# Kernel optimization log

Hardware: AMD Instinct MI355X
Metric: run time of the kernel (lower is better)

## Reference

```python
import jax, jax.numpy as jnp
import numpy as np
import math

H = 2048      # hidden_size
NH = 16       # num_attention_heads
HN = H // NH  # head dim = 128
B = 4
S = 2048

def setup_inputs() -> dict:
    key = jax.random.key(0)
    k1, k2, k3, k4, k5 = jax.random.split(key, 5)
    hidden_states = jax.random.normal(k1, (B, S, H), dtype=jnp.float32)
    # causal (left-to-right) multiplicative mask, [1,1,s,s]
    ltor_mask = jnp.tril(jnp.ones((S, S), dtype=jnp.float32))[None, None]
    scale = 0.02
    w_qkv = jax.random.normal(k2, (H, 3 * H), dtype=jnp.float32) * scale
    b_qkv = jnp.zeros((3 * H,), dtype=jnp.float32)
    w_dense = jax.random.normal(k3, (H, H), dtype=jnp.float32) * scale
    b_dense = jnp.zeros((H,), dtype=jnp.float32)
    return {"hidden_states": hidden_states, "ltor_mask": ltor_mask,
            "w_qkv": w_qkv, "b_qkv": b_qkv, "w_dense": w_dense, "b_dense": b_dense}

def reference(hidden_states, ltor_mask, w_qkv, b_qkv, w_dense, b_dense):
    b, s, h = hidden_states.shape
    mixed = hidden_states @ w_qkv + b_qkv                      # [b,s,3h]
    q, k, v = jnp.split(mixed, 3, axis=-1)                     # each [b,s,h]
    def heads(t):
        return t.reshape(b, s, NH, HN).transpose(0, 2, 1, 3)   # [b,np,s,hn]
    q, k, v = heads(q), heads(k), heads(v)
    scores = jnp.einsum('bnqd,bnkd->bnqk', q, k) / math.sqrt(HN)
    scores = scores * ltor_mask - 10000.0 * (1.0 - ltor_mask)
    probs = jax.nn.softmax(scores, axis=-1)
    # dropout probs are 0 -> identity
    ctx = jnp.einsum('bnqk,bnkd->bnqd', probs, v)               # [b,np,s,hn]
    ctx = ctx.transpose(0, 2, 1, 3).reshape(b, s, h)            # [b,s,h]
    out = ctx @ w_dense + b_dense
    return out
```

## Files before the change

### kernel.cpp

```cpp
#include <hip/hip_runtime.h>

#define NHEADS 16
#define HDIM 2048
#define HN 128
#define SS 2048

typedef short short8 __attribute__((ext_vector_type(8)));
typedef __bf16 bf16x8 __attribute__((ext_vector_type(8)));
typedef float f32x4 __attribute__((ext_vector_type(4)));

__device__ __forceinline__ unsigned short f2bf(float f) {
  unsigned int u = __float_as_uint(f);
  u += 0x7FFFu + ((u >> 16) & 1u);
  return (unsigned short)(u >> 16);
}
__device__ __forceinline__ bf16x8 ld8(const void* p) {
  short8 s = *(const short8*)p;
  return __builtin_bit_cast(bf16x8, s);
}
__device__ __forceinline__ void gld_lds16(const void* g, void* l) {
  __builtin_amdgcn_global_load_lds(
      (const __attribute__((address_space(1))) unsigned int*)g,
      (__attribute__((address_space(3))) unsigned int*)l, 16, 0, 0);
}

__global__ __launch_bounds__(256) void cast_bf16_kernel(
    const float* __restrict__ in, unsigned short* __restrict__ out, int n4) {
  int i = blockIdx.x * 256 + threadIdx.x;
  if (i >= n4) return;
  float4 v = ((const float4*)in)[i];
  ushort4 o;
  o.x = f2bf(v.x); o.y = f2bf(v.y); o.z = f2bf(v.z); o.w = f2bf(v.w);
  ((ushort4*)out)[i] = o;
}

__global__ __launch_bounds__(256) void transpose_cast_kernel(
    const float* __restrict__ in, unsigned short* __restrict__ out, int R, int C) {
  __shared__ float tile[64][65];
  int tx = threadIdx.x & 63, ty = threadIdx.x >> 6;
  int c0 = blockIdx.x * 64, r0 = blockIdx.y * 64;
#pragma unroll
  for (int i = 0; i < 16; ++i) {
    int r = ty + i * 4;
    tile[r][tx] = in[(size_t)(r0 + r) * C + (c0 + tx)];
  }
  __syncthreads();
#pragma unroll
  for (int i = 0; i < 16; ++i) {
    int r = ty + i * 4;
    out[(size_t)(c0 + r) * R + (r0 + tx)] = f2bf(tile[tx][r]);
  }
}


#define STAGE_A(bsel, h, kt)                                                      \
  do {                                                                            \
    gld_lds16((const char*)(Ab + (size_t)sa_m[h][0] * K + (size_t)(kt) * 64) +    \
                  scol0,                                                          \
              lds + (bsel) * 65536 + (h) * 16384 + t * 16);                       \
    gld_lds16((const char*)(Ab + (size_t)sa_m[h][1] * K + (size_t)(kt) * 64) +    \
                  scol1,                                                          \
              lds + (bsel) * 65536 + (h) * 16384 + (t + 512) * 16);               \
  } while (0)

#define STAGE_B(bsel, h, kt)                                                      \
  do {                                                                            \
    gld_lds16((const char*)(Bb + (size_t)sb_n[h][0] * K + (size_t)(kt) * 64) +    \
                  scol0,                                                          \
              lds + (bsel) * 65536 + 32768 + (h) * 16384 + t * 16);               \
    gld_lds16((const char*)(Bb + (size_t)sb_n[h][1] * K + (size_t)(kt) * 64) +    \
                  scol1,                                                          \
              lds + (bsel) * 65536 + 32768 + (h) * 16384 + (t + 512) * 16);       \
  } while (0)

#define LDA(bsel, mh)                                                             \
  do {                                                                            \
    _Pragma("unroll") for (int mf = 0; mf < 4; ++mf) {                            \
      int row = mf * 16 + ln15 + wr * 64 + (mh) * 128;                            \
      int sw = (row & 7) << 4;                                                    \
      const char* base = lds + (bsel) * 65536 + row * 128;                        \
      a[mf][0] = ld8(base + ((g * 16) ^ sw));                                     \
      a[mf][1] = ld8(base + ((64 + g * 16) ^ sw));                                \
    }                                                                             \
  } while (0)

#define LDB(bsel, nh, breg)                                                       \
  do {                                                                            \
    _Pragma("unroll") for (int nf = 0; nf < 2; ++nf) {                            \
      int row = nf * 16 + ln15 + wc * 32 + (nh) * 128;                            \
      int sw = (row & 7) << 4;                                                    \
      const char* base = lds + (bsel) * 65536 + 32768 + row * 128;                \
      breg[nf][0] = ld8(base + ((g * 16) ^ sw));                                  \
      breg[nf][1] = ld8(base + ((64 + g * 16) ^ sw));                             \
    }                                                                             \
  } while (0)

#define QMFMA(mh, nh, breg)                                                       \
  do {                                                                            \
    __builtin_amdgcn_s_setprio(1);                                                \
    _Pragma("unroll") for (int mf = 0; mf < 4; ++mf)                              \
        _Pragma("unroll") for (int nf = 0; nf < 2; ++nf)                          \
            _Pragma("unroll") for (int ks = 0; ks < 2; ++ks)                      \
                acc[(mh) * 4 + mf][(nh) * 2 + nf] =                               \
        __builtin_amdgcn_mfma_f32_16x16x32_bf16(                                  \
            a[mf][ks], breg[nf][ks], acc[(mh) * 4 + mf][(nh) * 2 + nf], 0, 0, 0); \
    __builtin_amdgcn_s_setprio(0);                                                \
  } while (0)

#define BARRIER asm volatile("s_barrier" ::: "memory")
#define VMCNT(n) asm volatile("s_waitcnt vmcnt(" #n ")" ::: "memory")

template <int EPI>
__global__ __launch_bounds__(512, 2) void gemm256_kernel(
    const unsigned short* __restrict__ A, const unsigned short* __restrict__ Bt,
    const float* __restrict__ bias, float* __restrict__ Of,
    unsigned short* __restrict__ Oq, unsigned short* __restrict__ Ok,
    unsigned short* __restrict__ Ovt, int M, int N, int K) {
  __shared__ __align__(16) char lds[131072];
  const int t = threadIdx.x;
  const int lane = t & 63, wid = t >> 6;
  const int wr = wid >> 2, wc = wid & 3;
  const int g = lane >> 4, ln15 = lane & 15;
  const int brow = blockIdx.y * 256, bcol = blockIdx.x * 256;
  const unsigned short* Ab = A + (size_t)brow * K;
  const unsigned short* Bb = Bt + (size_t)bcol * K;

  int r0 = t >> 3, r1 = (t + 512) >> 3;
  const int scol0 = ((t & 7) * 16) ^ ((r0 & 7) << 4);
  const int scol1 = (((t + 512) & 7) * 16) ^ ((r1 & 7) << 4);
  int sa_m[2][2], sb_n[2][2];
#pragma unroll
  for (int h = 0; h < 2; ++h) {
    int ra = h * 128 + r0, rb = h * 128 + r1;
    sa_m[h][0] = (ra & 63) + ((ra >> 6) & 1) * 128 + ((ra >> 7) & 1) * 64;
    sa_m[h][1] = (rb & 63) + ((rb >> 6) & 1) * 128 + ((rb >> 7) & 1) * 64;
    sb_n[h][0] = (ra & 31) + ((ra >> 5) & 3) * 64 + ((ra >> 7) & 1) * 32;
    sb_n[h][1] = (rb & 31) + ((rb >> 5) & 3) * 64 + ((rb >> 7) & 1) * 32;
  }

  f32x4 acc[8][4];
#pragma unroll
  for (int m = 0; m < 8; ++m)
#pragma unroll
    for (int n = 0; n < 4; ++n) acc[m][n] = (f32x4){0.f, 0.f, 0.f, 0.f};
  bf16x8 a[4][2], b0[2][2], b1[2][2];

  const int nt = K >> 6;
  STAGE_A(0, 0, 0);
  STAGE_B(0, 0, 0);
  STAGE_B(0, 1, 0);
  STAGE_A(0, 1, 0);
  STAGE_A(1, 0, 1);
  VMCNT(6);
  BARRIER;

  for (int tk = 0; tk < nt - 1; ++tk) {
    const int bsel = tk & 1, bnext = bsel ^ 1;
    LDA(bsel, 0);
    LDB(bsel, 0, b0);
    STAGE_B(bnext, 0, tk + 1);
    BARRIER;
    QMFMA(0, 0, b0);
    VMCNT(6);
    BARRIER;
    LDB(bsel, 1, b1);
    STAGE_B(bnext, 1, tk + 1);
    BARRIER;
    QMFMA(0, 1, b1);
    VMCNT(6);
    BARRIER;
    LDA(bsel, 1);
    STAGE_A(bnext, 1, tk + 1);
    BARRIER;
    QMFMA(1, 0, b0);
    BARRIER;
    if (tk + 2 < nt) STAGE_A(bsel, 0, tk + 2);
    BARRIER;
    QMFMA(1, 1, b1);
    if (tk < nt - 2) { VMCNT(6); } else { VMCNT(4); }
    BARRIER;
  }
  {
    const int bsel = (nt - 1) & 1;
    LDA(bsel, 0);
    LDB(bsel, 0, b0);
    BARRIER;
    QMFMA(0, 0, b0);
    VMCNT(2);
    BARRIER;
    LDB(bsel, 1, b1);
    BARRIER;
    QMFMA(0, 1, b1);
    VMCNT(0);
    BARRIER;
    LDA(bsel, 1);
    BARRIER;
    QMFMA(1, 0, b0);
    BARRIER;
    QMFMA(1, 1, b1);
  }

  if (EPI == 0) {
    const int which = bcol >> 11;
#pragma unroll
    for (int mf = 0; mf < 8; ++mf) {
      int rbase = brow + wr * 128 + mf * 16 + g * 4;
      int b = rbase >> 11, s = rbase & 2047;
#pragma unroll
      for (int nf = 0; nf < 4; ++nf) {
        int cglob = bcol + wc * 64 + nf * 16 + ln15;
        float bv = bias[cglob];
        int head = (cglob >> 7) & 15;
        int d = cglob & 127;
        if (which == 2) {
          ushort4 pk;
          pk.x = f2bf(acc[mf][nf][0] + bv);
          pk.y = f2bf(acc[mf][nf][1] + bv);
          pk.z = f2bf(acc[mf][nf][2] + bv);
          pk.w = f2bf(acc[mf][nf][3] + bv);
          *(ushort4*)&Ovt[((size_t)(b * NHEADS + head) * HN + d) * SS + s] = pk;
        } else {
          unsigned short* dst = which ? Ok : Oq;
#pragma unroll
          for (int j = 0; j < 4; ++j)
            dst[((size_t)(b * NHEADS + head) * SS + (s + j)) * HN + d] =
                f2bf(acc[mf][nf][j] + bv);
        }
      }
    }
  } else {
#pragma unroll
    for (int mf = 0; mf < 8; ++mf) {
      int rbase = brow + wr * 128 + mf * 16 + g * 4;
#pragma unroll
      for (int nf = 0; nf < 4; ++nf) {
        int cglob = bcol + wc * 64 + nf * 16 + ln15;
        float bv = bias[cglob];
#pragma unroll
        for (int j = 0; j < 4; ++j)
          Of[(size_t)(rbase + j) * N + cglob] = acc[mf][nf][j] + bv;
      }
    }
  }
}

__global__ __launch_bounds__(256, 2) void attn_kernel(
    const unsigned short* __restrict__ Q, const unsigned short* __restrict__ Kb,
    const unsigned short* __restrict__ Vt, unsigned short* __restrict__ ctx) {
  __shared__ __align__(16) unsigned short Klds[64 * 128];
  __shared__ __align__(16) unsigned short Vlds[128 * 64];
  __shared__ __align__(16) unsigned short Plds[4][32 * 72];
  int t = threadIdx.x, lane = t & 63, wid = t >> 6;
  int g = lane >> 4, ln15 = lane & 15;
  int qi = (int)(gridDim.x - 1) - (int)blockIdx.x;
  int bh = blockIdx.y;
  int q0 = qi * 128;
  int qbase = q0 + wid * 32;
  const unsigned short* Qb = Q + (size_t)bh * SS * HN;
  const unsigned short* Kbh = Kb + (size_t)bh * SS * HN;
  const unsigned short* Vtb = Vt + (size_t)bh * HN * SS;

  bf16x8 qf[2][4];
#pragma unroll
  for (int mr = 0; mr < 2; ++mr) {
    int qrow = qbase + mr * 16 + ln15;
#pragma unroll
    for (int dsi = 0; dsi < 4; ++dsi)
      qf[mr][dsi] = ld8(Qb + (size_t)qrow * HN + dsi * 32 + g * 8);
  }
  f32x4 o[2][8];
#pragma unroll
  for (int mr = 0; mr < 2; ++mr)
#pragma unroll
    for (int n = 0; n < 8; ++n) o[mr][n] = (f32x4){0.f, 0.f, 0.f, 0.f};
  float m_run[2][4], l_run[2][4];
#pragma unroll
  for (int mr = 0; mr < 2; ++mr)
#pragma unroll
    for (int j = 0; j < 4; ++j) { m_run[mr][j] = -1e30f; l_run[mr][j] = 0.f; }
  const float scale = 0.08838834764831845f;
  unsigned short* Pw = Plds[wid];

  int nkt = 2 * qi + 2;
  for (int kt = 0; kt < nkt; ++kt) {
    int k0 = kt * 64;
    __syncthreads();
    {
      const char* Ks = (const char*)(Kbh + (size_t)k0 * HN);
#pragma unroll
      for (int i = 0; i < 4; ++i) {
        int c = t + i * 256;
        int sb = (c * 16) ^ (((c >> 4) & 7) << 4);
        gld_lds16(Ks + sb, (char*)Klds + c * 16);
      }
    }
    {
#pragma unroll
      for (int i = 0; i < 4; ++i) {
        int c = t + i * 256;
        int row = c >> 3;
        int colsw = ((c & 7) * 16) ^ ((row & 7) << 4);
        gld_lds16((const char*)(Vtb + (size_t)row * SS + k0) + colsw,
                  (char*)Vlds + c * 16);
      }
    }
    __syncthreads();
    bool active = (k0 <= qbase + 31);
    if (active) {
      f32x4 sacc[2][4];
#pragma unroll
      for (int mr = 0; mr < 2; ++mr)
#pragma unroll
        for (int f = 0; f < 4; ++f) sacc[mr][f] = (f32x4){0.f, 0.f, 0.f, 0.f};
      __builtin_amdgcn_s_setprio(1);
#pragma unroll
      for (int f = 0; f < 4; ++f) {
        int keyl = f * 16 + ln15;
        int swzk = (keyl & 7) << 4;
#pragma unroll
        for (int dsi = 0; dsi < 4; ++dsi) {
          int off = (keyl * 256 + (dsi * 32 + g * 8) * 2) ^ swzk;
          bf16x8 kf = ld8((const char*)Klds + off);
          sacc[0][f] = __builtin_amdgcn_mfma_f32_16x16x32_bf16(qf[0][dsi], kf, sacc[0][f], 0, 0, 0);
          sacc[1][f] = __builtin_amdgcn_mfma_f32_16x16x32_bf16(qf[1][dsi], kf, sacc[1][f], 0, 0, 0);
        }
      }
      __builtin_amdgcn_s_setprio(0);
      float resc[2][4], rs[2][4];
#pragma unroll
      for (int mr = 0; mr < 2; ++mr) {
        bool needmask = (k0 + 63) > (qbase + mr * 16);
        float pm[4];
#pragma unroll
        for (int j = 0; j < 4; ++j) pm[j] = -1e30f;
#pragma unroll
        for (int f = 0; f < 4; ++f) {
          int key_g = k0 + f * 16 + ln15;
#pragma unroll
          for (int j = 0; j < 4; ++j) {
            float s = sacc[mr][f][j] * scale;
            if (needmask) {
              int q_g = qbase + mr * 16 + g * 4 + j;
              if (key_g > q_g) s = -1e30f;
            }
            sacc[mr][f][j] = s;
            pm[j] = fmaxf(pm[j], s);
          }
        }
#pragma unroll
        for (int j = 0; j < 4; ++j) {
          float v = pm[j];
          v = fmaxf(v, __shfl_xor(v, 1, 16));
          v = fmaxf(v, __shfl_xor(v, 2, 16));
          v = fmaxf(v, __shfl_xor(v, 4, 16));
          v = fmaxf(v, __shfl_xor(v, 8, 16));
          float mn = fmaxf(m_run[mr][j], v);
          resc[mr][j] = __expf(m_run[mr][j] - mn);
          m_run[mr][j] = mn;
          rs[mr][j] = 0.f;
        }
#pragma unroll
        for (int f = 0; f < 4; ++f) {
#pragma unroll
          for (int j = 0; j < 4; ++j) {
            float p = __expf(sacc[mr][f][j] - m_run[mr][j]);
            rs[mr][j] += p;
            Pw[(mr * 16 + g * 4 + j) * 72 + f * 16 + ln15] = f2bf(p);
          }
        }
#pragma unroll
        for (int j = 0; j < 4; ++j) {
          float v = rs[mr][j];
          v += __shfl_xor(v, 1, 16);
          v += __shfl_xor(v, 2, 16);
          v += __shfl_xor(v, 4, 16);
          v += __shfl_xor(v, 8, 16);
          l_run[mr][j] = l_run[mr][j] * resc[mr][j] + v;
        }
#pragma unroll
        for (int n = 0; n < 8; ++n)
#pragma unroll
          for (int j = 0; j < 4; ++j) o[mr][n][j] *= resc[mr][j];
      }
#pragma unroll
      for (int ks = 0; ks < 2; ++ks) {
        bf16x8 pa0 = ld8(&Pw[(size_t)(ln15)*72 + ks * 32 + g * 8]);
        bf16x8 pa1 = ld8(&Pw[(size_t)(16 + ln15) * 72 + ks * 32 + g * 8]);
        __builtin_amdgcn_s_setprio(1);
#pragma unroll
        for (int n = 0; n < 8; ++n) {
          int d = n * 16 + ln15;
          int off = (d * 128 + ks * 64 + g * 16) ^ ((d & 7) << 4);
          bf16x8 vf = ld8((const char*)Vlds + off);
          o[0][n] = __builtin_amdgcn_mfma_f32_16x16x32_bf16(pa0, vf, o[0][n], 0, 0, 0);
          o[1][n] = __builtin_amdgcn_mfma_f32_16x16x32_bf16(pa1, vf, o[1][n], 0, 0, 0);
        }
        __builtin_amdgcn_s_setprio(0);
      }
    }
  }
  int b = bh >> 4, head = bh & 15;
#pragma unroll
  for (int mr = 0; mr < 2; ++mr)
#pragma unroll
    for (int j = 0; j < 4; ++j) {
      int qg = qbase + mr * 16 + g * 4 + j;
      float inv = 1.0f / l_run[mr][j];
      size_t base = ((size_t)(b * SS + qg)) * HDIM + head * HN + ln15;
#pragma unroll
      for (int n = 0; n < 8; ++n)
        ctx[base + n * 16] = f2bf(o[mr][n][j] * inv);
    }
}

extern "C" void kernel_launch(void* const* d_in, const int* in_sizes, int n_in,
                              void* d_out, int out_size, void* d_ws, size_t ws_size,
                              hipStream_t stream) {
  const float* hs = (const float*)d_in[0];
  const float* w_qkv = (const float*)d_in[2];
  const float* b_qkv = (const float*)d_in[3];
  const float* w_dense = (const float*)d_in[4];
  const float* b_dense = (const float*)d_in[5];
  float* out = (float*)d_out;

  char* ws = (char*)d_ws;
  unsigned short* hsb   = (unsigned short*)(ws);
  unsigned short* wqkvT = (unsigned short*)(ws + 33554432);
  unsigned short* qb    = (unsigned short*)(ws + 58720256);
  unsigned short* kb    = (unsigned short*)(ws + 92274688);
  unsigned short* vtb   = (unsigned short*)(ws + 125829120);
  unsigned short* ctxb  = hsb;
  unsigned short* wdT   = wqkvT;

  cast_bf16_kernel<<<16384, 256, 0, stream>>>(hs, hsb, 4194304);
  transpose_cast_kernel<<<dim3(96, 32), 256, 0, stream>>>(w_qkv, wqkvT, 2048, 6144);
  gemm256_kernel<0><<<dim3(24, 32), 512, 0, stream>>>(
      hsb, wqkvT, b_qkv, nullptr, qb, kb, vtb, 8192, 6144, 2048);
  transpose_cast_kernel<<<dim3(32, 32), 256, 0, stream>>>(w_dense, wdT, 2048, 2048);
  attn_kernel<<<dim3(16, 64), 256, 0, stream>>>(qb, kb, vtb, ctxb);
  gemm256_kernel<1><<<dim3(8, 32), 512, 0, stream>>>(
      ctxb, wdT, b_dense, out, nullptr, nullptr, nullptr, 8192, 2048, 2048);
}
```

Before: 679.3 us.

## Prefetch next K/V tile into registers to overlap loads with attention compute

Replaces direct global-to-LDS loads of K and V tiles with register prefetching. The loads for the next tile are issued right after the current tile is written to LDS, so global memory latency overlaps the QK^T, softmax and PV compute. Swizzle offsets are precomputed once per thread. This costs 32 extra VGPRs per thread under launch_bounds(256,2), which may raise register pressure or cause spills, and it adds explicit LDS stores.

```diff
diff --git a/kernel.cpp b/kernel.cpp
--- a/kernel.cpp
+++ b/kernel.cpp
@@ -51,7 +51,6 @@
     out[(size_t)(c0 + r) * R + (r0 + tx)] = f2bf(tile[tx][r]);
   }
 }
-
 
 #define STAGE_A(bsel, h, kt)                                                      \
   do {                                                                            \
@@ -260,6 +259,16 @@
   const unsigned short* Kbh = Kb + (size_t)bh * SS * HN;
   const unsigned short* Vtb = Vt + (size_t)bh * HN * SS;
 
+  int kc[4], ksb[4], vrow[4], vcsw[4];
+#pragma unroll
+  for (int i = 0; i < 4; ++i) {
+    int c = t + i * 256;
+    kc[i] = c;
+    ksb[i] = (c * 16) ^ (((c >> 4) & 7) << 4);
+    vrow[i] = c >> 3;
+    vcsw[i] = ((c & 7) * 16) ^ (((c >> 3) & 7) << 4);
+  }
+
   bf16x8 qf[2][4];
 #pragma unroll
   for (int mr = 0; mr < 2; ++mr) {
@@ -281,30 +290,29 @@
   const float scale = 0.08838834764831845f;
   unsigned short* Pw = Plds[wid];
 
+  uint4 kreg[4], vreg[4];
+  auto issue_loads = [&](int k0n) {
+    const char* Ks = (const char*)(Kbh + (size_t)k0n * HN);
+#pragma unroll
+    for (int i = 0; i < 4; ++i)
+      kreg[i] = *(const uint4*)(Ks + ksb[i]);
+#pragma unroll
+    for (int i = 0; i < 4; ++i)
+      vreg[i] = *(const uint4*)((const char*)(Vtb + (size_t)vrow[i] * SS + k0n) + vcsw[i]);
+  };
+
   int nkt = 2 * qi + 2;
+  issue_loads(0);
   for (int kt = 0; kt < nkt; ++kt) {
     int k0 = kt * 64;
     __syncthreads();
-    {
-      const char* Ks = (const char*)(Kbh + (size_t)k0 * HN);
-#pragma unroll
-      for (int i = 0; i < 4; ++i) {
-        int c = t + i * 256;
-        int sb = (c * 16) ^ (((c >> 4) & 7) << 4);
-        gld_lds16(Ks + sb, (char*)Klds + c * 16);
-      }
-    }
-    {
-#pragma unroll
-      for (int i = 0; i < 4; ++i) {
-        int c = t + i * 256;
-        int row = c >> 3;
-        int colsw = ((c & 7) * 16) ^ ((row & 7) << 4);
-        gld_lds16((const char*)(Vtb + (size_t)row * SS + k0) + colsw,
-                  (char*)Vlds + c * 16);
-      }
+#pragma unroll
+    for (int i = 0; i < 4; ++i) {
+      *(uint4*)((char*)Klds + kc[i] * 16) = kreg[i];
+      *(uint4*)((char*)Vlds + kc[i] * 16) = vreg[i];
     }
     __syncthreads();
+    if (kt + 1 < nkt) issue_loads(k0 + 64);
     bool active = (k0 <= qbase + 31);
     if (active) {
       f32x4 sacc[2][4];
```

Measured after the change: 788.0 us. +16.0%, slower.
